# Optimization experiments

Measured on AMD Instinct MI355X. Metric: run time of the kernel, lower is better.

## Reference

```python
import jax, jax.numpy as jnp
import numpy as np

N_NODES = 20000
N_EDGES = 8192
UNITS = 128
NUM_GAUSSIANS = 50
CUTOFF = 8.0
GAMMA = 10.0
MIN_DIST, MAX_DIST = 0.0, 30.0


def setup_inputs() -> dict:
    key = jax.random.key(0)
    ks = jax.random.split(key, 6)
    node_features = jax.random.normal(ks[0], (N_NODES, UNITS), dtype=jnp.float32)
    edge_indices = jax.random.randint(ks[1], (2, N_EDGES), 0, N_NODES, dtype=jnp.int32)
    distances = jax.random.uniform(ks[2], (N_EDGES,), dtype=jnp.float32)
    # filter network params (Dense(units) -> swish -> Dense(units*units))
    W1 = jax.random.normal(ks[3], (NUM_GAUSSIANS, UNITS), dtype=jnp.float32) / np.sqrt(NUM_GAUSSIANS)
    b1 = jnp.zeros((UNITS,), dtype=jnp.float32)
    W2 = jax.random.normal(ks[4], (UNITS, UNITS * UNITS), dtype=jnp.float32) / np.sqrt(UNITS)
    b2 = jnp.zeros((UNITS * UNITS,), dtype=jnp.float32)
    # transform Dense(units, use_bias=False)
    Wt = jax.random.normal(ks[5], (UNITS, UNITS), dtype=jnp.float32) / np.sqrt(UNITS)
    return {"node_features": node_features, "edge_indices": edge_indices,
            "distances": distances, "W1": W1, "b1": b1, "W2": W2, "b2": b2, "Wt": Wt}


def reference(node_features, edge_indices, distances, W1, b1, W2, b2, Wt):
    n_nodes, units = node_features.shape
    # cutoff mask (multiplicative; dropped edges contribute zero to the scatter-sum,
    # equivalent to tf.boolean_mask + unsorted_segment_sum)
    mask = (distances <= CUTOFF).astype(node_features.dtype)  # [E]
    # Gaussian basis expansion
    centers = jnp.linspace(MIN_DIST, MAX_DIST, NUM_GAUSSIANS, dtype=jnp.float32)
    df = jnp.exp(-GAMMA * jnp.square(distances[:, None] - centers[None, :]))  # [E, G]
    # filter network: Dense -> swish -> Dense(units*units)
    h = jax.nn.silu(df @ W1 + b1)                    # [E, U]
    filters = (h @ W2 + b2).reshape(-1, units, units)  # [E, U, U]
    # gather source node features, transform, per-edge matvec
    src = node_features[edge_indices[0]]             # [E, U]
    transformed = src @ Wt                           # [E, U]
    filtered = jnp.einsum('eij,ej->ei', filters, transformed) * mask[:, None]  # [E, U]
    # scatter-sum to destination nodes
    messages = jax.ops.segment_sum(filtered, edge_indices[1], num_segments=n_nodes)
    return jax.nn.silu(messages)
```

## Files before the change

kernel.cpp:

```cpp
#include <hip/hip_runtime.h>
#include <hip/hip_fp16.h>


typedef _Float16 f16;
typedef __attribute__((ext_vector_type(8))) f16 f16x8;
typedef __attribute__((ext_vector_type(4))) float f32x4;
typedef __attribute__((ext_vector_type(4))) unsigned int u32x4;

#define NEDGE 8192
#define NNODE 20000
#define NG    50
#define KSTEPS 516
#define W2C_BYTES (KSTEPS * 8192)
#define HT_BYTES (64 * 132 * 128 * 2)
#define TM_BYTES (NEDGE * 128 * 2)
#define FP_BYTES ((size_t)8 * NEDGE * 128 * 4)

#define LDS_H   0
#define LDS_TM  5120
#define LDS_TOT 37888

static __device__ __forceinline__ float fsilu(float x) { return x / (1.0f + __expf(-x)); }

static __device__ __forceinline__ void gll16(const void* g, void* l) {
  __builtin_amdgcn_global_load_lds(
      (const __attribute__((address_space(1))) unsigned int*)g,
      (__attribute__((address_space(3))) unsigned int*)l, 16, 0, 0);
}

__global__ __launch_bounds__(256) void k01(const float* __restrict__ W2,
                                           const float* __restrict__ b2,
                                           const float* __restrict__ NF,
                                           const int*   __restrict__ EI,
                                           const float* __restrict__ DI,
                                           const float* __restrict__ W1,
                                           const float* __restrict__ B1,
                                           const float* __restrict__ WT,
                                           f16* __restrict__ w2c,
                                           f16* __restrict__ ht2,
                                           f16* __restrict__ tmo,
                                           float* __restrict__ out, int nz4) {
  __shared__ union {
    f16 row[16384];
    struct {
      float df[16][NG]; float mask[16]; float src[16][128];
      float tt[16][132]; float ht[16][132];
    } k1;
  } sm;
  const int bid = blockIdx.x, tid = threadIdx.x;

  if (bid < 129) {
    const int u = bid;
    const float* src = (u < 128) ? (W2 + (size_t)u * 16384) : b2;
#pragma unroll
    for (int it = 0; it < 16; ++it) {
      int idx = it * 1024 + tid * 4;
      f32x4 v = *(const f32x4*)(src + idx);
#pragma unroll
      for (int r = 0; r < 4; ++r) sm.row[idx + r] = (f16)v[r];
    }
    __syncthreads();
#pragma unroll
    for (int q = 0; q < 8; ++q) {
      int fi = q * 256 + tid;
      int lane = fi & 63, nt = (fi >> 6) & 7, s = fi >> 9;
      int i = nt * 16 + (lane & 15);
      int j = s * 32 + (lane >> 4) * 8;
      u32x4 frag = *(const u32x4*)&sm.row[i * 128 + j];
      *((u32x4*)w2c + (size_t)(u * 4 + s) * 512 + nt * 64 + lane) = frag;
    }
    return;
  }
  if (bid < 641) {
    int et = bid - 129, e0 = et * 16;
    for (int idx = tid; idx < 16 * NG; idx += 256) {
      int e = idx / NG, g = idx - e * NG;
      float d = DI[e0 + e];
      float x = d - (float)g * (30.0f / 49.0f);
      sm.k1.df[e][g] = __expf(-10.0f * x * x);
    }
    if (tid < 16) sm.k1.mask[tid] = (DI[e0 + tid] <= 8.0f) ? 1.0f : 0.0f;
    for (int idx = tid; idx < 16 * 128; idx += 256) {
      int e = idx >> 7, u = idx & 127;
      sm.k1.src[e][u] = NF[(size_t)EI[e0 + e] * 128 + u];
    }
    __syncthreads();

    int j = tid & 127, es = tid >> 7;
    for (int e = es * 8; e < es * 8 + 8; ++e) {
      float acc = B1[j];
      for (int g = 0; g < NG; ++g) acc += sm.k1.df[e][g] * W1[g * 128 + j];
      sm.k1.ht[e][j] = fsilu(acc);
    }
    {
      float acc[8] = {0.f,0.f,0.f,0.f,0.f,0.f,0.f,0.f};
      for (int u = 0; u < 128; ++u) {
        float wv = WT[u * 128 + j];
#pragma unroll
        for (int e8 = 0; e8 < 8; ++e8) acc[e8] += sm.k1.src[es * 8 + e8][u] * wv;
      }
#pragma unroll
      for (int e8 = 0; e8 < 8; ++e8) sm.k1.tt[es * 8 + e8][j] = acc[e8];
    }
    __syncthreads();

    int eb = et >> 3, el0 = (et & 7) * 16;
    {
      int u = tid >> 1, hf = tid & 1;
      union { f16 s[8]; u32x4 v; } pk;
#pragma unroll
      for (int k = 0; k < 8; ++k) pk.s[k] = (f16)sm.k1.ht[hf * 8 + k][u];
      *(u32x4*)(ht2 + ((size_t)eb * 132 + u) * 128 + el0 + hf * 8) = pk.v;
    }
    if (tid < 16) ht2[((size_t)eb * 132 + 128) * 128 + el0 + tid] = (f16)1.0f;
    {
      int e = tid >> 4, cc = tid & 15;
      float m = sm.k1.mask[e];
      union { f16 s[8]; u32x4 v; } pk;
#pragma unroll
      for (int k = 0; k < 8; ++k) pk.s[k] = (f16)(m * sm.k1.tt[e][cc * 8 + k]);
      int col = (cc * 16) ^ ((e & 7) << 4);
      *(u32x4*)((char*)tmo + (size_t)(e0 + e) * 256 + col) = pk.v;
    }
    return;
  }
  {
    int base = (bid - 641) * 1024;
    f32x4 z = {0.f, 0.f, 0.f, 0.f};
#pragma unroll
    for (int k = 0; k < 4; ++k) {
      int i4 = base + k * 256 + tid;
      if (i4 < nz4) ((f32x4*)out)[i4] = z;
    }
  }
}

template<int MODE>
__global__ __launch_bounds__(256, 2) void k2_gemm(const f16* __restrict__ w2c,
                                                  const f16* __restrict__ ht2,
                                                  const f16* __restrict__ tm,
                                                  const int* __restrict__ EI,
                                                  float* __restrict__ fpart,
                                                  float* __restrict__ msg) {
  __shared__ u32x4 smem_v[LDS_TOT / 16];
  char* smem = (char*)smem_v;

  const int bid = blockIdx.x;
  const int c   = bid & 7;
  const int eb  = bid >> 3;
  const int e0  = eb * 128;
  const int nu  = (c == 7) ? 17 : 16;
  const int tid = threadIdx.x, w = tid >> 6, lane = tid & 63;
  const int l15 = lane & 15, g4 = lane >> 4;
  const int wm = w >> 1, wn = w & 1;

  {
    const char* tsrc = (const char*)tm + (size_t)e0 * 256 + w * 8192;
#pragma unroll
    for (int q = 0; q < 8; ++q)
      gll16(tsrc + q * 1024 + lane * 16,
            smem + LDS_TM + w * 8192 + q * 1024 + lane * 16);
  }
  if (w == 0) {
    const char* hsrc = (const char*)ht2 + ((size_t)eb * 132 + c * 16) * 256;
#pragma unroll
    for (int q = 0; q < 5; ++q)
      gll16(hsrc + q * 1024 + lane * 16, smem + LDS_H + q * 1024 + lane * 16);
  }
  __syncthreads();

  f16x8 Tall[4][4];
  {
    const int tmrow = LDS_TM + (wm * 64 + l15) * 256;
    const int colsw = (l15 & 7) << 4;
#pragma unroll
    for (int rt = 0; rt < 4; ++rt)
#pragma unroll
      for (int jc = 0; jc < 4; ++jc)
        Tall[rt][jc] = *(const f16x8*)(smem + tmrow + rt * 4096 +
                                       ((jc * 64 + g4 * 16) ^ colsw));
  }
  const __half* hbase = (const __half*)(smem + LDS_H) + wm * 64 + l15;

  __half2 hc[4], hn[4];
#pragma unroll
  for (int rt = 0; rt < 4; ++rt) hc[rt] = __half2half2(hbase[rt * 16]);

  const char* bp = (const char*)w2c + (size_t)(c * 64) * 8192 + wn * 4096 + lane * 16;
  f16x8 B0[4], B1[4];
#pragma unroll
  for (int nt = 0; nt < 4; ++nt) B0[nt] = *(const f16x8*)(bp + nt * 1024);
#pragma unroll
  for (int nt = 0; nt < 4; ++nt) B1[nt] = *(const f16x8*)(bp + 8192 + nt * 1024);
  size_t off = 2 * 8192;

  f32x4 acc[4][4];
#pragma unroll
  for (int rt = 0; rt < 4; ++rt)
#pragma unroll
    for (int nt = 0; nt < 4; ++nt) acc[rt][nt] = (f32x4){0.f, 0.f, 0.f, 0.f};

  for (int u = 0; u < nu; ++u) {
#pragma unroll
    for (int jc = 0; jc < 4; ++jc) {
      if (jc == 1) {
#pragma unroll
        for (int rt = 0; rt < 4; ++rt)
          hn[rt] = __half2half2(hbase[(u + 1) * 128 + rt * 16]);
      }
      union uf { f16x8 v; __half2 h[4]; };
      uf a[4];
#pragma unroll
      for (int rt = 0; rt < 4; ++rt) {
        uf t; t.v = Tall[rt][jc];
#pragma unroll
        for (int q = 0; q < 4; ++q) a[rt].h[q] = __hmul2(t.h[q], hc[rt]);
      }
      __builtin_amdgcn_s_setprio(1);
#pragma unroll
      for (int nt = 0; nt < 4; ++nt) {
        if ((jc & 1) == 0) {
#pragma unroll
          for (int rt = 0; rt < 4; ++rt)
            acc[rt][nt] = __builtin_amdgcn_mfma_f32_16x16x32_f16(a[rt].v, B0[nt], acc[rt][nt], 0, 0, 0);
          B0[nt] = *(const f16x8*)(bp + off + nt * 1024);
        } else {
#pragma unroll
          for (int rt = 0; rt < 4; ++rt)
            acc[rt][nt] = __builtin_amdgcn_mfma_f32_16x16x32_f16(a[rt].v, B1[nt], acc[rt][nt], 0, 0, 0);
          B1[nt] = *(const f16x8*)(bp + off + nt * 1024);
        }
      }
      __builtin_amdgcn_s_setprio(0);
      off += 8192;
    }
#pragma unroll
    for (int rt = 0; rt < 4; ++rt) hc[rt] = hn[rt];
  }

  if (MODE == 0) {
#pragma unroll
    for (int rt = 0; rt < 4; ++rt) {
#pragma unroll
      for (int r = 0; r < 4; ++r) {
        int e = e0 + wm * 64 + rt * 16 + g4 * 4 + r;
        float* prow = fpart + ((size_t)c * NEDGE + e) * 128 + wn * 64 + l15;
#pragma unroll
        for (int nt = 0; nt < 4; ++nt)
          prow[nt * 16] = acc[rt][nt][r];
      }
    }
  } else {
    const int* dst = EI + NEDGE;
#pragma unroll
    for (int rt = 0; rt < 4; ++rt) {
#pragma unroll
      for (int r = 0; r < 4; ++r) {
        int e = e0 + wm * 64 + rt * 16 + g4 * 4 + r;
        float* row = msg + (size_t)dst[e] * 128 + wn * 64 + l15;
#pragma unroll
        for (int nt = 0; nt < 4; ++nt)
          atomicAdd(row + nt * 16, acc[rt][nt][r]);
      }
    }
  }
}

__global__ __launch_bounds__(256) void k4_reduce(const float* __restrict__ fp,
                                                 const int* __restrict__ EI,
                                                 float* __restrict__ out) {
  int gid = blockIdx.x * 256 + threadIdx.x;
  int e  = gid >> 5;
  int i0 = (gid & 31) << 2;
  f32x4 s = {0.f, 0.f, 0.f, 0.f};
#pragma unroll
  for (int cc = 0; cc < 8; ++cc) {
    f32x4 v = *(const f32x4*)(fp + ((size_t)cc * NEDGE + e) * 128 + i0);
    s[0] += v[0]; s[1] += v[1]; s[2] += v[2]; s[3] += v[3];
  }
  float* row = out + (size_t)EI[NEDGE + e] * 128 + i0;
  atomicAdd(row + 0, s[0]);
  atomicAdd(row + 1, s[1]);
  atomicAdd(row + 2, s[2]);
  atomicAdd(row + 3, s[3]);
}

__global__ __launch_bounds__(256) void k3_silu(float* __restrict__ out, int n4) {
  int idx = blockIdx.x * 256 + threadIdx.x;
  int stride = gridDim.x * 256;
  f32x4* p = (f32x4*)out;
  for (; idx < n4; idx += stride) {
    f32x4 v = p[idx];
#pragma unroll
    for (int cc = 0; cc < 4; ++cc) v[cc] = fsilu(v[cc]);
    p[idx] = v;
  }
}

extern "C" void kernel_launch(void* const* d_in, const int* in_sizes, int n_in,
                              void* d_out, int out_size, void* d_ws, size_t ws_size,
                              hipStream_t stream) {
  const float* NF = (const float*)d_in[0];
  const int*   EI = (const int*)  d_in[1];
  const float* DI = (const float*)d_in[2];
  const float* W1 = (const float*)d_in[3];
  const float* B1 = (const float*)d_in[4];
  const float* W2 = (const float*)d_in[5];
  const float* B2 = (const float*)d_in[6];
  const float* WT = (const float*)d_in[7];
  float* out = (float*)d_out;

  f16*   w2c = (f16*)d_ws;
  f16*   ht2 = (f16*)((char*)d_ws + W2C_BYTES);
  f16*   tmo = (f16*)((char*)d_ws + W2C_BYTES + HT_BYTES);
  float* fp  = (float*)((char*)d_ws + W2C_BYTES + HT_BYTES + TM_BYTES);
  size_t need_min  = (size_t)W2C_BYTES + HT_BYTES + TM_BYTES;
  size_t need_fast = need_min + FP_BYTES;
  if (ws_size < need_min) return;
  const bool fast = (ws_size >= need_fast);

  int nz4 = out_size / 4;
  k01<<<dim3(1266), dim3(256), 0, stream>>>(W2, B2, NF, EI, DI, W1, B1, WT,
                                            w2c, ht2, tmo, out, nz4);
  if (fast) {
    k2_gemm<0><<<dim3(512),  dim3(256), 0, stream>>>(w2c, ht2, tmo, EI, fp, out);
    k4_reduce <<<dim3(1024), dim3(256), 0, stream>>>(fp, EI, out);
  } else {
    k2_gemm<1><<<dim3(512),  dim3(256), 0, stream>>>(w2c, ht2, tmo, EI, fp, out);
  }
  k3_silu<<<dim3(1024), dim3(256), 0, stream>>>(out, nz4);
}
```

Before: 85.18 us.

## Split per-edge prep into MFMA kernel with prepacked fp16 WT and W1 fragments

The per-edge filter-network first layer and the source-feature transform move out of the combined prep kernel. They now run in a new kernel that uses 16x16x32 fp16 MFMA with swizzled LDS tiles, replacing scalar fp32 loops. WT and W1 (with the bias folded in as an extra basis column) are prepacked into fp16 MFMA fragments in the first kernel. This adds one kernel launch and lowers the precision of these small GEMMs to fp16. In the main GEMM kernel, the W2 fragment loads are also hoisted ahead of the LDS staging.

After: 82.24 us. 1.04x faster.

```diff
diff --git a/kernel.cpp b/kernel.cpp
--- a/kernel.cpp
+++ b/kernel.cpp
@@ -14,11 +14,18 @@
 #define W2C_BYTES (KSTEPS * 8192)
 #define HT_BYTES (64 * 132 * 128 * 2)
 #define TM_BYTES (NEDGE * 128 * 2)
+#define WTC_BYTES (4 * 8 * 64 * 8 * 2)
+#define W1C_BYTES (2 * 8 * 64 * 8 * 2)
 #define FP_BYTES ((size_t)8 * NEDGE * 128 * 4)
 
 #define LDS_H   0
 #define LDS_TM  5120
 #define LDS_TOT 37888
+
+#define K1_SRC 0
+#define K1_DF  16384
+#define K1_MSK 24576
+#define K1_TOT 24832
 
 static __device__ __forceinline__ float fsilu(float x) { return x / (1.0f + __expf(-x)); }
 
@@ -28,25 +35,16 @@
       (__attribute__((address_space(3))) unsigned int*)l, 16, 0, 0);
 }
 
-__global__ __launch_bounds__(256) void k01(const float* __restrict__ W2,
-                                           const float* __restrict__ b2,
-                                           const float* __restrict__ NF,
-                                           const int*   __restrict__ EI,
-                                           const float* __restrict__ DI,
-                                           const float* __restrict__ W1,
-                                           const float* __restrict__ B1,
-                                           const float* __restrict__ WT,
-                                           f16* __restrict__ w2c,
-                                           f16* __restrict__ ht2,
-                                           f16* __restrict__ tmo,
-                                           float* __restrict__ out, int nz4) {
-  __shared__ union {
-    f16 row[16384];
-    struct {
-      float df[16][NG]; float mask[16]; float src[16][128];
-      float tt[16][132]; float ht[16][132];
-    } k1;
-  } sm;
+__global__ __launch_bounds__(256) void k0all(const float* __restrict__ W2,
+                                             const float* __restrict__ b2,
+                                             const float* __restrict__ W1,
+                                             const float* __restrict__ B1,
+                                             const float* __restrict__ WT,
+                                             f16* __restrict__ w2c,
+                                             f16* __restrict__ wtc,
+                                             f16* __restrict__ w1c,
+                                             float* __restrict__ out, int nz4) {
+  __shared__ f16 srow[16384];
   const int bid = blockIdx.x, tid = threadIdx.x;
 
   if (bid < 129) {
@@ -57,7 +55,7 @@
       int idx = it * 1024 + tid * 4;
       f32x4 v = *(const f32x4*)(src + idx);
 #pragma unroll
-      for (int r = 0; r < 4; ++r) sm.row[idx + r] = (f16)v[r];
+      for (int r = 0; r < 4; ++r) srow[idx + r] = (f16)v[r];
     }
     __syncthreads();
 #pragma unroll
@@ -66,66 +64,47 @@
       int lane = fi & 63, nt = (fi >> 6) & 7, s = fi >> 9;
       int i = nt * 16 + (lane & 15);
       int j = s * 32 + (lane >> 4) * 8;
-      u32x4 frag = *(const u32x4*)&sm.row[i * 128 + j];
+      u32x4 frag = *(const u32x4*)&srow[i * 128 + j];
       *((u32x4*)w2c + (size_t)(u * 4 + s) * 512 + nt * 64 + lane) = frag;
     }
     return;
   }
-  if (bid < 641) {
-    int et = bid - 129, e0 = et * 16;
-    for (int idx = tid; idx < 16 * NG; idx += 256) {
-      int e = idx / NG, g = idx - e * NG;
-      float d = DI[e0 + e];
-      float x = d - (float)g * (30.0f / 49.0f);
-      sm.k1.df[e][g] = __expf(-10.0f * x * x);
-    }
-    if (tid < 16) sm.k1.mask[tid] = (DI[e0 + tid] <= 8.0f) ? 1.0f : 0.0f;
-    for (int idx = tid; idx < 16 * 128; idx += 256) {
-      int e = idx >> 7, u = idx & 127;
-      sm.k1.src[e][u] = NF[(size_t)EI[e0 + e] * 128 + u];
-    }
-    __syncthreads();
-
-    int j = tid & 127, es = tid >> 7;
-    for (int e = es * 8; e < es * 8 + 8; ++e) {
-      float acc = B1[j];
-      for (int g = 0; g < NG; ++g) acc += sm.k1.df[e][g] * W1[g * 128 + j];
-      sm.k1.ht[e][j] = fsilu(acc);
-    }
-    {
-      float acc[8] = {0.f,0.f,0.f,0.f,0.f,0.f,0.f,0.f};
-      for (int u = 0; u < 128; ++u) {
-        float wv = WT[u * 128 + j];
-#pragma unroll
-        for (int e8 = 0; e8 < 8; ++e8) acc[e8] += sm.k1.src[es * 8 + e8][u] * wv;
-      }
-#pragma unroll
-      for (int e8 = 0; e8 < 8; ++e8) sm.k1.tt[es * 8 + e8][j] = acc[e8];
-    }
-    __syncthreads();
-
-    int eb = et >> 3, el0 = (et & 7) * 16;
-    {
-      int u = tid >> 1, hf = tid & 1;
+  if (bid < 133) {
+    int step = bid - 129;
+#pragma unroll
+    for (int q = 0; q < 2; ++q) {
+      int fi = q * 256 + tid;
+      int lane = fi & 63, nt = fi >> 6;
+      int j = nt * 16 + (lane & 15);
       union { f16 s[8]; u32x4 v; } pk;
 #pragma unroll
-      for (int k = 0; k < 8; ++k) pk.s[k] = (f16)sm.k1.ht[hf * 8 + k][u];
-      *(u32x4*)(ht2 + ((size_t)eb * 132 + u) * 128 + el0 + hf * 8) = pk.v;
-    }
-    if (tid < 16) ht2[((size_t)eb * 132 + 128) * 128 + el0 + tid] = (f16)1.0f;
-    {
-      int e = tid >> 4, cc = tid & 15;
-      float m = sm.k1.mask[e];
+      for (int r = 0; r < 8; ++r) {
+        int u = step * 32 + (lane >> 4) * 8 + r;
+        pk.s[r] = (f16)WT[u * 128 + j];
+      }
+      *((u32x4*)wtc + (step * 8 + nt) * 64 + lane) = pk.v;
+    }
+    return;
+  }
+  if (bid == 133) {
+#pragma unroll
+    for (int q = 0; q < 4; ++q) {
+      int fi = q * 256 + tid;
+      int lane = fi & 63, nt = (fi >> 6) & 7, step = fi >> 9;
+      int j = nt * 16 + (lane & 15);
       union { f16 s[8]; u32x4 v; } pk;
 #pragma unroll
-      for (int k = 0; k < 8; ++k) pk.s[k] = (f16)(m * sm.k1.tt[e][cc * 8 + k]);
-      int col = (cc * 16) ^ ((e & 7) << 4);
-      *(u32x4*)((char*)tmo + (size_t)(e0 + e) * 256 + col) = pk.v;
+      for (int r = 0; r < 8; ++r) {
+        int g = step * 32 + (lane >> 4) * 8 + r;
+        float v = (g < 50) ? W1[g * 128 + j] : ((g == 63) ? B1[j] : 0.0f);
+        pk.s[r] = (f16)v;
+      }
+      *((u32x4*)w1c + (step * 8 + nt) * 64 + lane) = pk.v;
     }
     return;
   }
   {
-    int base = (bid - 641) * 1024;
+    int base = (bid - 134) * 1024;
     f32x4 z = {0.f, 0.f, 0.f, 0.f};
 #pragma unroll
     for (int k = 0; k < 4; ++k) {
@@ -133,6 +112,107 @@
       if (i4 < nz4) ((f32x4*)out)[i4] = z;
     }
   }
+}
+
+__global__ __launch_bounds__(256) void k1m(const float* __restrict__ NF,
+                                           const int*   __restrict__ EI,
+                                           const float* __restrict__ DI,
+                                           const f16* __restrict__ wtc,
+                                           const f16* __restrict__ w1c,
+                                           f16* __restrict__ ht2,
+                                           f16* __restrict__ tmo) {
+  __shared__ u32x4 smem_v[K1_TOT / 16];
+  char* smem = (char*)smem_v;
+  const int bid = blockIdx.x, tid = threadIdx.x;
+  const int e0g = bid * 64;
+  const int eb  = bid >> 1;
+  const int el0 = (bid & 1) * 64;
+
+  if (tid < 64) {
+    float d = DI[e0g + tid];
+    *(float*)(smem + K1_MSK + tid * 4) = (d <= 8.0f) ? 1.0f : 0.0f;
+  }
+  {
+    int e = tid >> 2, g0 = (tid & 3) * 16;
+    float d = DI[e0g + e];
+    union { f16 s[16]; u32x4 v[2]; } pk;
+#pragma unroll
+    for (int gg = 0; gg < 16; ++gg) {
+      int g = g0 + gg;
+      float x = d - (float)g * (30.0f / 49.0f);
+      float v = (g < 50) ? __expf(-10.0f * x * x) : ((g == 63) ? 1.0f : 0.0f);
+      pk.s[gg] = (f16)v;
+    }
+    int base = e * 128 + g0 * 2, sw = (e & 7) << 4;
+    *(u32x4*)(smem + K1_DF + ((base) ^ sw))      = pk.v[0];
+    *(u32x4*)(smem + K1_DF + ((base + 16) ^ sw)) = pk.v[1];
+  }
+#pragma unroll
+  for (int p = 0; p < 8; ++p) {
+    int e = p * 8 + (tid >> 5);
+    int u0 = (tid & 31) * 4;
+    int row = EI[e0g + e];
+    f32x4 v = *(const f32x4*)(NF + (size_t)row * 128 + u0);
+    union { f16 s[4]; unsigned long long q; } pk;
+#pragma unroll
+    for (int r = 0; r < 4; ++r) pk.s[r] = (f16)v[r];
+    int addr = e * 256 + u0 * 2;
+    *(unsigned long long*)(smem + K1_SRC + (addr ^ ((e & 7) << 4))) = pk.q;
+  }
+  __syncthreads();
+
+  const int w = tid >> 6, lane = tid & 63;
+  const int l15 = lane & 15, g4 = lane >> 4;
+  const int erow = w * 16;
+  const int asw = (l15 & 7) << 4;
+
+  f32x4 at[8], ah[8];
+#pragma unroll
+  for (int nt = 0; nt < 8; ++nt) {
+    at[nt] = (f32x4){0.f, 0.f, 0.f, 0.f};
+    ah[nt] = (f32x4){0.f, 0.f, 0.f, 0.f};
+  }
+  const f16x8* wtp = (const f16x8*)wtc;
+  const f16x8* w1p = (const f16x8*)w1c;
+
+#pragma unroll
+  for (int step = 0; step < 4; ++step) {
+    int aaddr = (erow + l15) * 256 + step * 64 + g4 * 16;
+    f16x8 a = *(const f16x8*)(smem + K1_SRC + (aaddr ^ asw));
+#pragma unroll
+    for (int nt = 0; nt < 8; ++nt)
+      at[nt] = __builtin_amdgcn_mfma_f32_16x16x32_f16(a, wtp[(step * 8 + nt) * 64 + lane], at[nt], 0, 0, 0);
+  }
+#pragma unroll
+  for (int step = 0; step < 2; ++step) {
+    int aaddr = (erow + l15) * 128 + step * 64 + g4 * 16;
+    f16x8 a = *(const f16x8*)(smem + K1_DF + (aaddr ^ asw));
+#pragma unroll
+    for (int nt = 0; nt < 8; ++nt)
+      ah[nt] = __builtin_amdgcn_mfma_f32_16x16x32_f16(a, w1p[(step * 8 + nt) * 64 + lane], ah[nt], 0, 0, 0);
+  }
+
+  const float* mk = (const float*)(smem + K1_MSK);
+#pragma unroll
+  for (int r = 0; r < 4; ++r) {
+    int el_ = erow + g4 * 4 + r;
+    float m = mk[el_];
+    int sw2 = (el_ & 7) << 4;
+    char* rowp = (char*)tmo + (size_t)(e0g + el_) * 256;
+#pragma unroll
+    for (int nt = 0; nt < 8; ++nt)
+      *(f16*)(rowp + (((nt * 16 + l15) * 2) ^ sw2)) = (f16)(m * at[nt][r]);
+  }
+#pragma unroll
+  for (int r = 0; r < 4; ++r) {
+    int el_ = el0 + erow + g4 * 4 + r;
+#pragma unroll
+    for (int nt = 0; nt < 8; ++nt) {
+      int u = nt * 16 + l15;
+      ht2[((size_t)eb * 132 + u) * 128 + el_] = (f16)fsilu(ah[nt][r]);
+    }
+  }
+  if (tid < 64) ht2[((size_t)eb * 132 + 128) * 128 + el0 + tid] = (f16)1.0f;
 }
 
 template<int MODE>
@@ -154,6 +234,13 @@
   const int l15 = lane & 15, g4 = lane >> 4;
   const int wm = w >> 1, wn = w & 1;
 
+  const char* bp = (const char*)w2c + (size_t)(c * 64) * 8192 + wn * 4096 + lane * 16;
+  f16x8 B0[4], B1[4];
+#pragma unroll
+  for (int nt = 0; nt < 4; ++nt) B0[nt] = *(const f16x8*)(bp + nt * 1024);
+#pragma unroll
+  for (int nt = 0; nt < 4; ++nt) B1[nt] = *(const f16x8*)(bp + 8192 + nt * 1024);
+
   {
     const char* tsrc = (const char*)tm + (size_t)e0 * 256 + w * 8192;
 #pragma unroll
@@ -186,14 +273,7 @@
 #pragma unroll
   for (int rt = 0; rt < 4; ++rt) hc[rt] = __half2half2(hbase[rt * 16]);
 
-  const char* bp = (const char*)w2c + (size_t)(c * 64) * 8192 + wn * 4096 + lane * 16;
-  f16x8 B0[4], B1[4];
-#pragma unroll
-  for (int nt = 0; nt < 4; ++nt) B0[nt] = *(const f16x8*)(bp + nt * 1024);
-#pragma unroll
-  for (int nt = 0; nt < 4; ++nt) B1[nt] = *(const f16x8*)(bp + 8192 + nt * 1024);
   size_t off = 2 * 8192;
-
   f32x4 acc[4][4];
 #pragma unroll
   for (int rt = 0; rt < 4; ++rt)
@@ -310,18 +390,21 @@
   const float* WT = (const float*)d_in[7];
   float* out = (float*)d_out;
 
-  f16*   w2c = (f16*)d_ws;
-  f16*   ht2 = (f16*)((char*)d_ws + W2C_BYTES);
-  f16*   tmo = (f16*)((char*)d_ws + W2C_BYTES + HT_BYTES);
-  float* fp  = (float*)((char*)d_ws + W2C_BYTES + HT_BYTES + TM_BYTES);
-  size_t need_min  = (size_t)W2C_BYTES + HT_BYTES + TM_BYTES;
+  char* base = (char*)d_ws;
+  f16*   w2c = (f16*)base;
+  f16*   ht2 = (f16*)(base + W2C_BYTES);
+  f16*   tmo = (f16*)(base + W2C_BYTES + HT_BYTES);
+  f16*   wtc = (f16*)(base + W2C_BYTES + HT_BYTES + TM_BYTES);
+  f16*   w1c = (f16*)(base + W2C_BYTES + HT_BYTES + TM_BYTES + WTC_BYTES);
+  float* fp  = (float*)(base + W2C_BYTES + HT_BYTES + TM_BYTES + WTC_BYTES + W1C_BYTES);
+  size_t need_min  = (size_t)W2C_BYTES + HT_BYTES + TM_BYTES + WTC_BYTES + W1C_BYTES;
   size_t need_fast = need_min + FP_BYTES;
   if (ws_size < need_min) return;
   const bool fast = (ws_size >= need_fast);
 
   int nz4 = out_size / 4;
-  k01<<<dim3(1266), dim3(256), 0, stream>>>(W2, B2, NF, EI, DI, W1, B1, WT,
-                                            w2c, ht2, tmo, out, nz4);
+  k0all<<<dim3(759), dim3(256), 0, stream>>>(W2, B2, W1, B1, WT, w2c, wtc, w1c, out, nz4);
+  k1m  <<<dim3(128), dim3(256), 0, stream>>>(NF, EI, DI, wtc, w1c, ht2, tmo);
   if (fast) {
     k2_gemm<0><<<dim3(512),  dim3(256), 0, stream>>>(w2c, ht2, tmo, EI, fp, out);
     k4_reduce <<<dim3(1024), dim3(256), 0, stream>>>(fp, EI, out);
```
